# Kernel optimization log

Hardware: AMD Instinct MI355X
Metric: run time of the kernel (lower is better)

Reference implementation:

```python
import jax, jax.numpy as jnp
import numpy as np

N_IN = 1024
N_OUT = 1024
BATCH = 8192
N_GRID = 10  # grid_points = linspace(-1, 1, 10); 9 segments
LN_EPS = 1e-5


def setup_inputs() -> dict:
    key = jax.random.key(0)
    k = jax.random.split(key, 6)
    return {
        "x": jax.random.normal(k[0], (BATCH, N_IN), dtype=jnp.float32),
        "weights": jax.random.normal(k[1], (N_OUT, N_IN), dtype=jnp.float32) * (1.0 / np.sqrt(N_IN)),
        "biases": jax.random.normal(k[2], (N_OUT,), dtype=jnp.float32),
        "slopes": jax.random.normal(k[3], (N_OUT, N_IN, N_GRID - 1), dtype=jnp.float32) * 0.05,
        "intercepts": jax.random.normal(k[4], (N_OUT, N_IN, N_GRID - 1), dtype=jnp.float32) * 0.05,
        "prelu_weight": jnp.full((1,), 0.25, dtype=jnp.float32),
    }


def reference(x, weights, biases, slopes, intercepts, prelu_weight):
    grid = jnp.linspace(-1.0, 1.0, N_GRID, dtype=x.dtype)
    n_seg = N_GRID - 1

    # base branch: GELU (exact, matching torch nn.GELU default) then linear
    b_out = jax.nn.gelu(x, approximate=False) @ weights.T + biases  # [B, n_out]

    # segment index per (sample, input feature)
    pos = (x[..., None] - grid) >= 0  # [B, n_in, N_GRID]
    seg = jnp.clip(jnp.sum(pos.astype(jnp.int32), axis=-1) - 1, 0, n_seg - 1)  # [B, n_in]

    # Faithful to torch.gather semantics: only slopes[:, 0, :] / intercepts[:, 0, :]
    # are read (index dim-2 has size 1 -> j==0). The piecewise sum over n_in then
    # reduces to segment-sums of x and segment counts contracted with those slices.
    onehot = jax.nn.one_hot(seg, n_seg, dtype=x.dtype)  # [B, n_in, n_seg]
    seg_x = jnp.einsum('bis,bi->bs', onehot, x)          # sum of x per segment
    seg_cnt = jnp.sum(onehot, axis=1)                    # count per segment
    slopes0 = slopes[:, 0, :]        # [n_out, n_seg]
    icpt0 = intercepts[:, 0, :]      # [n_out, n_seg]
    lin = seg_x @ slopes0.T + seg_cnt @ icpt0.T          # [B, n_out]

    y = b_out + lin
    # LayerNorm over n_out, no affine
    mu = jnp.mean(y, axis=-1, keepdims=True)
    var = jnp.mean(jnp.square(y - mu), axis=-1, keepdims=True)
    yn = (y - mu) * jax.lax.rsqrt(var + LN_EPS)
    # PReLU with single shared weight
    return jnp.where(yn >= 0, yn, prelu_weight * yn)
```

## Files before the change

### kernel.cpp

```cpp
#include <hip/hip_runtime.h>

#define N_IN 1024
#define N_OUT 1024
#define BATCHN 8192
#define BK 64

typedef __attribute__((ext_vector_type(8))) short short8;
typedef __attribute__((ext_vector_type(4))) float floatx4;

__device__ __forceinline__ unsigned short f2bf(float f) {
  unsigned int u = __float_as_uint(f);
  u += 0x7FFFu + ((u >> 16) & 1u);
  return (unsigned short)(u >> 16);
}

__global__ __launch_bounds__(256) void prep_all(const float* __restrict__ x,
                                                unsigned short* __restrict__ g,
                                                float* __restrict__ seg,
                                                const float* __restrict__ W,
                                                unsigned short* __restrict__ Wb,
                                                const float* __restrict__ slopes,
                                                const float* __restrict__ icpts,
                                                float* __restrict__ slt,
                                                float* __restrict__ ict) {
  const int b = blockIdx.x;
  const int t = threadIdx.x;
  if (b < BATCHN / 4) {
    const int lane = t & 63, wv = t >> 6;
    const int row = b * 4 + wv;
    const float* xr = x + row * N_IN;
    unsigned short* gr = g + row * N_IN;
    float lx[9], lc[9];
#pragma unroll
    for (int s = 0; s < 9; ++s) { lx[s] = 0.f; lc[s] = 0.f; }
#pragma unroll
    for (int j = 0; j < 4; ++j) {
      float4 v4 = ((const float4*)xr)[lane + 64 * j];
      float vs[4] = {v4.x, v4.y, v4.z, v4.w};
      ushort4 o4;
#pragma unroll
      for (int e = 0; e < 4; ++e) {
        float v = vs[e];
        float gl = 0.5f * v * (1.0f + erff(v * 0.70710678f));
        ((unsigned short*)&o4)[e] = f2bf(gl);
        int cnt = 0;
#pragma unroll
        for (int k = 0; k < 10; ++k)
          cnt += (v >= (-1.0f + (float)k * (2.0f / 9.0f))) ? 1 : 0;
        int sg = cnt - 1;
        sg = sg < 0 ? 0 : (sg > 8 ? 8 : sg);
#pragma unroll
        for (int s = 0; s < 9; ++s) {
          lx[s] += (sg == s) ? v : 0.0f;
          lc[s] += (sg == s) ? 1.0f : 0.0f;
        }
      }
      ((ushort4*)gr)[lane + 64 * j] = o4;
    }
#pragma unroll
    for (int s = 0; s < 9; ++s) {
#pragma unroll
      for (int off = 32; off > 0; off >>= 1) {
        lx[s] += __shfl_xor(lx[s], off);
        lc[s] += __shfl_xor(lc[s], off);
      }
    }
    if (lane == 0) {
#pragma unroll
      for (int s = 0; s < 9; ++s) {
        seg[row * 18 + s] = lx[s];
        seg[row * 18 + 9 + s] = lc[s];
      }
    }
  } else if (b < BATCHN / 4 + N_OUT) {
    const int o = b - BATCHN / 4;
    float4 v = ((const float4*)(W + o * N_IN))[t];
    ushort4 u;
    u.x = f2bf(v.x);
    u.y = f2bf(v.y);
    u.z = f2bf(v.z);
    u.w = f2bf(v.w);
    ((ushort4*)(Wb + o * N_IN))[t] = u;
  } else {
    const int gb = b - (BATCHN / 4 + N_OUT);
    const int o = gb * 16 + (t >> 4);
    const int s = t & 15;
    if (s < 9) {
      slt[s * N_OUT + o] = slopes[(long)o * 9216 + s];
      ict[s * N_OUT + o] = icpts[(long)o * 9216 + s];
    }
  }
}

#define ASYNC_CP16(gp, lp)                                                     \
  __builtin_amdgcn_global_load_lds(                                            \
      (const __attribute__((address_space(1))) unsigned int*)(gp),             \
      (__attribute__((address_space(3))) unsigned int*)(lp), 16, 0, 0)

__global__ __launch_bounds__(256) void gemm_bt(const unsigned short* __restrict__ A,
                                               const unsigned short* __restrict__ B,
                                               float* __restrict__ C) {
  __shared__ unsigned short lA[128 * BK];
  __shared__ unsigned short lB[128 * BK];
  const int t = threadIdx.x;
  const int m0 = blockIdx.x * 128;
  const int n0 = blockIdx.y * 128;
  const int lane = t & 63, wv = t >> 6;
  const int wm = (wv >> 1) * 64, wn = (wv & 1) * 64;
  floatx4 acc[4][4] = {};

  const int arow = wm + (lane & 15);
  const int brow = wn + (lane & 15);
  const int kq = lane >> 4;

  for (int kt = 0; kt < N_IN / BK; ++kt) {
    __syncthreads();
    const int ko = kt * BK;
#pragma unroll
    for (int j = 0; j < 4; ++j) {
      const int sg = t + 256 * j;
      const int r = sg >> 3;
      const int l = (sg & 7) ^ (r & 7);
      ASYNC_CP16(A + (m0 + r) * N_IN + ko + l * 8, &lA[sg * 8]);
    }
#pragma unroll
    for (int j = 0; j < 4; ++j) {
      const int sg = t + 256 * j;
      const int r = sg >> 3;
      const int l = (sg & 7) ^ (r & 7);
      ASYNC_CP16(B + (n0 + r) * N_IN + ko + l * 8, &lB[sg * 8]);
    }
    __syncthreads();
#pragma unroll
    for (int kk = 0; kk < 2; ++kk) {
      short8 af[4], bf[4];
#pragma unroll
      for (int i = 0; i < 4; ++i) {
        const int row = arow + i * 16;
        const int pc = (kk * 4 + kq) ^ (row & 7);
        af[i] = *(const short8*)&lA[row * BK + pc * 8];
      }
#pragma unroll
      for (int i = 0; i < 4; ++i) {
        const int row = brow + i * 16;
        const int pc = (kk * 4 + kq) ^ (row & 7);
        bf[i] = *(const short8*)&lB[row * BK + pc * 8];
      }
#pragma unroll
      for (int mi = 0; mi < 4; ++mi)
#pragma unroll
        for (int ni = 0; ni < 4; ++ni)
          acc[mi][ni] = __builtin_amdgcn_mfma_f32_16x16x32_bf16(af[mi], bf[ni],
                                                                acc[mi][ni], 0, 0, 0);
    }
  }

  const int crow0 = m0 + wm + (lane >> 4) * 4;
  const int ccol0 = n0 + wn + (lane & 15);
#pragma unroll
  for (int mi = 0; mi < 4; ++mi)
#pragma unroll
    for (int ni = 0; ni < 4; ++ni)
#pragma unroll
      for (int rg = 0; rg < 4; ++rg)
        C[(crow0 + mi * 16 + rg) * N_OUT + ccol0 + ni * 16] = acc[mi][ni][rg];
}

__global__ __launch_bounds__(512) void ln_prelu(float* __restrict__ C,
                                                const float* __restrict__ biases,
                                                const float* __restrict__ seg,
                                                const float* __restrict__ slt,
                                                const float* __restrict__ ict,
                                                const float* __restrict__ prelu_w) {
  const int t = threadIdx.x;
  const int o1 = t, o2 = t + 512;
  const int lane = t & 63, wv = t >> 6;
  const float b1 = biases[o1], b2 = biases[o2];
  float sl1[9], sl2[9], ic1[9], ic2[9];
#pragma unroll
  for (int s = 0; s < 9; ++s) {
    sl1[s] = slt[s * N_OUT + o1];
    sl2[s] = slt[s * N_OUT + o2];
    ic1[s] = ict[s * N_OUT + o1];
    ic2[s] = ict[s * N_OUT + o2];
  }
  const float pw = prelu_w[0];
  __shared__ float2 red[2][8];
  for (int r = 0; r < 8; ++r) {
    const int row = blockIdx.x * 8 + r;
    const float* segr = seg + row * 18;
    float y1 = C[row * N_OUT + o1] + b1;
    float y2 = C[row * N_OUT + o2] + b2;
#pragma unroll
    for (int s = 0; s < 9; ++s) {
      float sx = segr[s], ct = segr[9 + s];
      y1 += sx * sl1[s] + ct * ic1[s];
      y2 += sx * sl2[s] + ct * ic2[s];
    }
    float sum = y1 + y2;
    float sq = y1 * y1 + y2 * y2;
#pragma unroll
    for (int off = 32; off > 0; off >>= 1) {
      sum += __shfl_xor(sum, off);
      sq += __shfl_xor(sq, off);
    }
    if (lane == 0) red[r & 1][wv] = make_float2(sum, sq);
    __syncthreads();
    float s8 = 0.f, q8 = 0.f;
#pragma unroll
    for (int i = 0; i < 8; ++i) {
      s8 += red[r & 1][i].x;
      q8 += red[r & 1][i].y;
    }
    const float mu = s8 * (1.0f / 1024.0f);
    const float var = q8 * (1.0f / 1024.0f) - mu * mu;
    const float rstd = rsqrtf(var + 1e-5f);
    float z1 = (y1 - mu) * rstd, z2 = (y2 - mu) * rstd;
    z1 = z1 >= 0.f ? z1 : pw * z1;
    z2 = z2 >= 0.f ? z2 : pw * z2;
    C[row * N_OUT + o1] = z1;
    C[row * N_OUT + o2] = z2;
  }
}

extern "C" void kernel_launch(void* const* d_in, const int* in_sizes, int n_in,
                              void* d_out, int out_size, void* d_ws, size_t ws_size,
                              hipStream_t stream) {
  const float* x = (const float*)d_in[0];
  const float* W = (const float*)d_in[1];
  const float* biases = (const float*)d_in[2];
  const float* slopes = (const float*)d_in[3];
  const float* icpts = (const float*)d_in[4];
  const float* prelu_w = (const float*)d_in[5];
  float* C = (float*)d_out;

  char* ws = (char*)d_ws;
  unsigned short* g = (unsigned short*)ws;
  unsigned short* Wb = (unsigned short*)(ws + (16u << 20));
  float* seg = (float*)(ws + (18u << 20));
  float* slt = (float*)(ws + (19u << 20));
  float* ict = (float*)(ws + (19u << 20) + (64u << 10));

  prep_all<<<BATCHN / 4 + N_OUT + 64, 256, 0, stream>>>(x, g, seg, W, Wb, slopes,
                                                        icpts, slt, ict);
  gemm_bt<<<dim3(BATCHN / 128, N_OUT / 128), 256, 0, stream>>>(g, Wb, C);
  ln_prelu<<<BATCHN / 8, 512, 0, stream>>>(C, biases, seg, slt, ict, prelu_w);
}
```

Baseline: 191.0 us.

## Store GEMM output as bf16, use 32x32 MFMA, cumulative segment sums

The GEMM intermediate is written to a bf16 workspace buffer instead of fp32 in the output, halving the bytes written by the GEMM and read by the LayerNorm kernel. The GEMM switches from 16x16x32 to 32x32x16 MFMA tiles, which changes the fragment loads and the epilogue mapping. The prep kernel computes segment sums through cumulative threshold counts, with fewer per-element ops and shuffles. Rounding the pre-LayerNorm activations to bf16 adds precision loss, and the epilogue writes scattered 2-byte stores.

```diff
diff --git a/kernel.cpp b/kernel.cpp
--- a/kernel.cpp
+++ b/kernel.cpp
@@ -6,12 +6,15 @@
 #define BK 64
 
 typedef __attribute__((ext_vector_type(8))) short short8;
-typedef __attribute__((ext_vector_type(4))) float floatx4;
+typedef __attribute__((ext_vector_type(16))) float floatx16;
 
 __device__ __forceinline__ unsigned short f2bf(float f) {
   unsigned int u = __float_as_uint(f);
   u += 0x7FFFu + ((u >> 16) & 1u);
   return (unsigned short)(u >> 16);
+}
+__device__ __forceinline__ float bf2f(unsigned short s) {
+  return __uint_as_float(((unsigned int)s) << 16);
 }
 
 __global__ __launch_bounds__(256) void prep_all(const float* __restrict__ x,
@@ -30,9 +33,9 @@
     const int row = b * 4 + wv;
     const float* xr = x + row * N_IN;
     unsigned short* gr = g + row * N_IN;
-    float lx[9], lc[9];
-#pragma unroll
-    for (int s = 0; s < 9; ++s) { lx[s] = 0.f; lc[s] = 0.f; }
+    float cum[8], cumx[8], totx = 0.f;
+#pragma unroll
+    for (int s = 0; s < 8; ++s) { cum[s] = 0.f; cumx[s] = 0.f; }
 #pragma unroll
     for (int j = 0; j < 4; ++j) {
       float4 v4 = ((const float4*)xr)[lane + 64 * j];
@@ -43,33 +46,40 @@
         float v = vs[e];
         float gl = 0.5f * v * (1.0f + erff(v * 0.70710678f));
         ((unsigned short*)&o4)[e] = f2bf(gl);
-        int cnt = 0;
-#pragma unroll
-        for (int k = 0; k < 10; ++k)
-          cnt += (v >= (-1.0f + (float)k * (2.0f / 9.0f))) ? 1 : 0;
-        int sg = cnt - 1;
-        sg = sg < 0 ? 0 : (sg > 8 ? 8 : sg);
-#pragma unroll
-        for (int s = 0; s < 9; ++s) {
-          lx[s] += (sg == s) ? v : 0.0f;
-          lc[s] += (sg == s) ? 1.0f : 0.0f;
+        totx += v;
+#pragma unroll
+        for (int k = 0; k < 8; ++k) {
+          bool m = v >= (-1.0f + (float)(k + 1) * (2.0f / 9.0f));
+          cum[k] += m ? 1.0f : 0.0f;
+          cumx[k] += m ? v : 0.0f;
         }
       }
       ((ushort4*)gr)[lane + 64 * j] = o4;
     }
 #pragma unroll
-    for (int s = 0; s < 9; ++s) {
-#pragma unroll
-      for (int off = 32; off > 0; off >>= 1) {
-        lx[s] += __shfl_xor(lx[s], off);
-        lc[s] += __shfl_xor(lc[s], off);
+    for (int off = 32; off > 0; off >>= 1) {
+      totx += __shfl_xor(totx, off);
+#pragma unroll
+      for (int s = 0; s < 8; ++s) {
+        cum[s] += __shfl_xor(cum[s], off);
+        cumx[s] += __shfl_xor(cumx[s], off);
       }
     }
     if (lane == 0) {
+      float sx[9], sc[9];
+      sx[0] = totx - cumx[0];
+      sc[0] = 1024.f - cum[0];
+#pragma unroll
+      for (int s = 1; s < 8; ++s) {
+        sx[s] = cumx[s - 1] - cumx[s];
+        sc[s] = cum[s - 1] - cum[s];
+      }
+      sx[8] = cumx[7];
+      sc[8] = cum[7];
 #pragma unroll
       for (int s = 0; s < 9; ++s) {
-        seg[row * 18 + s] = lx[s];
-        seg[row * 18 + 9 + s] = lc[s];
+        seg[row * 18 + s] = sx[s];
+        seg[row * 18 + 9 + s] = sc[s];
       }
     }
   } else if (b < BATCHN / 4 + N_OUT) {
@@ -99,7 +109,7 @@
 
 __global__ __launch_bounds__(256) void gemm_bt(const unsigned short* __restrict__ A,
                                                const unsigned short* __restrict__ B,
-                                               float* __restrict__ C) {
+                                               unsigned short* __restrict__ Cb) {
   __shared__ unsigned short lA[128 * BK];
   __shared__ unsigned short lB[128 * BK];
   const int t = threadIdx.x;
@@ -107,11 +117,10 @@
   const int n0 = blockIdx.y * 128;
   const int lane = t & 63, wv = t >> 6;
   const int wm = (wv >> 1) * 64, wn = (wv & 1) * 64;
-  floatx4 acc[4][4] = {};
-
-  const int arow = wm + (lane & 15);
-  const int brow = wn + (lane & 15);
-  const int kq = lane >> 4;
+  floatx16 acc[2][2] = {};
+
+  const int l31 = lane & 31;
+  const int lh = lane >> 5;
 
   for (int kt = 0; kt < N_IN / BK; ++kt) {
     __syncthreads();
@@ -132,41 +141,43 @@
     }
     __syncthreads();
 #pragma unroll
-    for (int kk = 0; kk < 2; ++kk) {
-      short8 af[4], bf[4];
-#pragma unroll
-      for (int i = 0; i < 4; ++i) {
-        const int row = arow + i * 16;
-        const int pc = (kk * 4 + kq) ^ (row & 7);
-        af[i] = *(const short8*)&lA[row * BK + pc * 8];
-      }
-#pragma unroll
-      for (int i = 0; i < 4; ++i) {
-        const int row = brow + i * 16;
-        const int pc = (kk * 4 + kq) ^ (row & 7);
-        bf[i] = *(const short8*)&lB[row * BK + pc * 8];
-      }
-#pragma unroll
-      for (int mi = 0; mi < 4; ++mi)
-#pragma unroll
-        for (int ni = 0; ni < 4; ++ni)
-          acc[mi][ni] = __builtin_amdgcn_mfma_f32_16x16x32_bf16(af[mi], bf[ni],
+    for (int kk = 0; kk < 4; ++kk) {
+      const int kc = kk * 2 + lh;
+      short8 af[2], bf[2];
+#pragma unroll
+      for (int i = 0; i < 2; ++i) {
+        const int row = wm + i * 32 + l31;
+        af[i] = *(const short8*)&lA[row * BK + ((kc ^ (row & 7)) * 8)];
+      }
+#pragma unroll
+      for (int i = 0; i < 2; ++i) {
+        const int row = wn + i * 32 + l31;
+        bf[i] = *(const short8*)&lB[row * BK + ((kc ^ (row & 7)) * 8)];
+      }
+#pragma unroll
+      for (int mi = 0; mi < 2; ++mi)
+#pragma unroll
+        for (int ni = 0; ni < 2; ++ni)
+          acc[mi][ni] = __builtin_amdgcn_mfma_f32_32x32x16_bf16(af[mi], bf[ni],
                                                                 acc[mi][ni], 0, 0, 0);
     }
   }
 
-  const int crow0 = m0 + wm + (lane >> 4) * 4;
-  const int ccol0 = n0 + wn + (lane & 15);
-#pragma unroll
-  for (int mi = 0; mi < 4; ++mi)
-#pragma unroll
-    for (int ni = 0; ni < 4; ++ni)
-#pragma unroll
-      for (int rg = 0; rg < 4; ++rg)
-        C[(crow0 + mi * 16 + rg) * N_OUT + ccol0 + ni * 16] = acc[mi][ni][rg];
-}
-
-__global__ __launch_bounds__(512) void ln_prelu(float* __restrict__ C,
+  const int lrow = 4 * lh;
+#pragma unroll
+  for (int mi = 0; mi < 2; ++mi)
+#pragma unroll
+    for (int ni = 0; ni < 2; ++ni)
+#pragma unroll
+      for (int rg = 0; rg < 16; ++rg) {
+        const int r = m0 + wm + mi * 32 + (rg & 3) + 8 * (rg >> 2) + lrow;
+        const int c = n0 + wn + ni * 32 + l31;
+        Cb[r * N_OUT + c] = f2bf(acc[mi][ni][rg]);
+      }
+}
+
+__global__ __launch_bounds__(512) void ln_prelu(const unsigned short* __restrict__ Cb,
+                                                float* __restrict__ out,
                                                 const float* __restrict__ biases,
                                                 const float* __restrict__ seg,
                                                 const float* __restrict__ slt,
@@ -189,8 +200,8 @@
   for (int r = 0; r < 8; ++r) {
     const int row = blockIdx.x * 8 + r;
     const float* segr = seg + row * 18;
-    float y1 = C[row * N_OUT + o1] + b1;
-    float y2 = C[row * N_OUT + o2] + b2;
+    float y1 = bf2f(Cb[row * N_OUT + o1]) + b1;
+    float y2 = bf2f(Cb[row * N_OUT + o2]) + b2;
 #pragma unroll
     for (int s = 0; s < 9; ++s) {
       float sx = segr[s], ct = segr[9 + s];
@@ -218,8 +229,8 @@
     float z1 = (y1 - mu) * rstd, z2 = (y2 - mu) * rstd;
     z1 = z1 >= 0.f ? z1 : pw * z1;
     z2 = z2 >= 0.f ? z2 : pw * z2;
-    C[row * N_OUT + o1] = z1;
-    C[row * N_OUT + o2] = z2;
+    out[row * N_OUT + o1] = z1;
+    out[row * N_OUT + o2] = z2;
   }
 }
 
@@ -232,17 +243,18 @@
   const float* slopes = (const float*)d_in[3];
   const float* icpts = (const float*)d_in[4];
   const float* prelu_w = (const float*)d_in[5];
-  float* C = (float*)d_out;
+  float* out = (float*)d_out;
 
   char* ws = (char*)d_ws;
   unsigned short* g = (unsigned short*)ws;
   unsigned short* Wb = (unsigned short*)(ws + (16u << 20));
-  float* seg = (float*)(ws + (18u << 20));
-  float* slt = (float*)(ws + (19u << 20));
-  float* ict = (float*)(ws + (19u << 20) + (64u << 10));
+  unsigned short* Cb = (unsigned short*)(ws + (18u << 20));
+  float* seg = (float*)(ws + (34u << 20));
+  float* slt = (float*)(ws + (35u << 20));
+  float* ict = (float*)(ws + (35u << 20) + (64u << 10));
 
   prep_all<<<BATCHN / 4 + N_OUT + 64, 256, 0, stream>>>(x, g, seg, W, Wb, slopes,
                                                         icpts, slt, ict);
-  gemm_bt<<<dim3(BATCHN / 128, N_OUT / 128), 256, 0, stream>>>(g, Wb, C);
-  ln_prelu<<<BATCHN / 8, 512, 0, stream>>>(C, biases, seg, slt, ict, prelu_w);
-}
+  gemm_bt<<<dim3(BATCHN / 128, N_OUT / 128), 256, 0, stream>>>(g, Wb, Cb);
+  ln_prelu<<<BATCHN / 8, 512, 0, stream>>>(Cb, out, biases, seg, slt, ict, prelu_w);
+}
```

After: 184.4 us. 1.04x faster.
